# Performance work log

Hardware: AMD Instinct MI355X
Metric: run time of the kernel (lower is better)

Reference implementation:

```python
import jax, jax.numpy as jnp
import numpy as np

D_MODEL, FFN, N_EXP = 1024, 4096, 8
BS, L = 4, 2048


def setup_inputs() -> dict:
    key = jax.random.key(0)
    ks = jax.random.split(key, 7)
    s = 0.02
    return {
        "x": jax.random.normal(ks[0], (BS, L, D_MODEL), dtype=jnp.float32),
        "gate_w": s * jax.random.normal(ks[1], (D_MODEL, N_EXP), dtype=jnp.float32),
        "gate_b": jnp.zeros((N_EXP,), dtype=jnp.float32),
        "W1": s * jax.random.normal(ks[2], (N_EXP, D_MODEL, FFN), dtype=jnp.float32),
        "b1": jnp.zeros((N_EXP, FFN), dtype=jnp.float32),
        "W2": s * jax.random.normal(ks[3], (N_EXP, FFN, D_MODEL), dtype=jnp.float32),
        "b2": jnp.zeros((N_EXP, D_MODEL), dtype=jnp.float32),
    }


def reference(x, gate_w, gate_b, W1, b1, W2, b2):
    # gate logits [bs, l, E]; NOTE: original applies Softmax(dim=1) -> over seq dim
    logits = jnp.einsum("bld,de->ble", x, gate_w) + gate_b
    probs = jax.nn.softmax(logits, axis=1)  # faithful to nn.Softmax(dim=1)
    idx = jnp.argmax(probs, axis=-1)  # top-1 expert per token, [bs, l]
    # topk_weights are computed in the original but never applied to output.
    out = jnp.zeros_like(x)
    for e in range(N_EXP):  # fixed small expert loop (structurally distinct weights)
        h = jax.nn.gelu(jnp.einsum("bld,df->blf", x, W1[e]) + b1[e], approximate=False)
        y = jnp.einsum("blf,fd->bld", h, W2[e]) + b2[e]
        out = out + jnp.where((idx == e)[..., None], y, jnp.float32(0.0))
    return out
```

## Files before the change

kernel.cpp:

```cpp
#include <hip/hip_runtime.h>
#include <hip/hip_bf16.h>

typedef unsigned short u16;
typedef unsigned int u32;

using bf16x8 = __attribute__((ext_vector_type(8))) short;
using f32x4  = __attribute__((ext_vector_type(4))) float;

static constexpr int TOK  = 8192;
static constexpr int SEQ  = 2048;
static constexpr int DM   = 1024;
static constexpr int FF   = 4096;
static constexpr int NE   = 8;
static constexpr int MAXT = 72;
static constexpr int KS2  = 4;
static constexpr int NWG1 = MAXT * (FF/128);
static constexpr int NWG2 = MAXT * (DM/128) * KS2;

static constexpr size_t O_LOGITS = 0;
static constexpr size_t O_M      = 262144;
static constexpr size_t O_Z      = O_M + 128;
static constexpr size_t O_CNT    = O_Z + 128;
static constexpr size_t O_CUR    = O_CNT + 64;
static constexpr size_t O_OFF    = O_CUR + 64;
static constexpr size_t O_DESC   = 263168;
static constexpr size_t O_PERM   = 266240;
static constexpr size_t O_IDX    = 299008;
static constexpr size_t O_XG     = 524288;
static constexpr size_t O_W1T    = O_XG  + (size_t)TOK*DM*2;
static constexpr size_t O_W2T    = O_W1T + (size_t)NE*DM*FF*2;
static constexpr size_t O_H      = O_W2T + (size_t)NE*DM*FF*2;

__device__ __forceinline__ u16 f2bf(float f){
  __hip_bfloat16 h = __float2bfloat16(f);
  return *reinterpret_cast<u16*>(&h);
}

__device__ __forceinline__ void gld_lds16(const void* g, void* l){
  __builtin_amdgcn_global_load_lds((const __attribute__((address_space(1))) void*)g,
                                   (__attribute__((address_space(3))) void*)l, 16, 0, 0);
}

__device__ __forceinline__ float gelu_f(float v){
  float u = v * fmaf(v*v, 0.044715f, 1.0f) * 0.7978845608f;
  float ex = __builtin_amdgcn_exp2f(u * -2.885390082f);
  return v * __builtin_amdgcn_rcpf(1.0f + ex);
}

__global__ void k_gate(const float* __restrict__ x, const float* __restrict__ gw,
                       const float* __restrict__ gb, float* __restrict__ logits){
  __shared__ float sgw[NE*DM];
  for (int i = threadIdx.x; i < DM*NE; i += 256){
    int d = i >> 3, e = i & 7;
    sgw[e*DM + d] = gw[i];
  }
  __syncthreads();
  int wave = threadIdx.x >> 6, lane = threadIdx.x & 63;
  int t = blockIdx.x * 4 + wave;
  const float4* xr = (const float4*)(x + (size_t)t * DM);
  float acc[NE];
#pragma unroll
  for (int e = 0; e < NE; ++e) acc[e] = 0.f;
#pragma unroll
  for (int k = 0; k < 4; ++k){
    int v4 = k*64 + lane;
    float4 v = xr[v4];
#pragma unroll
    for (int e = 0; e < NE; ++e){
      const float4 g = *(const float4*)&sgw[e*DM + v4*4];
      acc[e] = fmaf(v.x, g.x, fmaf(v.y, g.y, fmaf(v.z, g.z, fmaf(v.w, g.w, acc[e]))));
    }
  }
#pragma unroll
  for (int off = 32; off; off >>= 1)
#pragma unroll
    for (int e = 0; e < NE; ++e) acc[e] += __shfl_xor(acc[e], off);
  if (lane == 0){
#pragma unroll
    for (int e = 0; e < NE; ++e) logits[(size_t)t*NE + e] = acc[e] + gb[e];
  }
}

__global__ void k_lse(const float* __restrict__ logits, float* __restrict__ mOut,
                      float* __restrict__ zOut){
  int be = blockIdx.x;
  int b = be >> 3, e = be & 7;
  const float* base = logits + ((size_t)b*SEQ)*NE + e;
  float m = -INFINITY;
  for (int l = threadIdx.x; l < SEQ; l += 256) m = fmaxf(m, base[(size_t)l*NE]);
  __shared__ float red[8];
#pragma unroll
  for (int off = 32; off; off >>= 1) m = fmaxf(m, __shfl_xor(m, off));
  if ((threadIdx.x & 63) == 0) red[threadIdx.x >> 6] = m;
  __syncthreads();
  m = fmaxf(fmaxf(red[0], red[1]), fmaxf(red[2], red[3]));
  float s = 0.f;
  for (int l = threadIdx.x; l < SEQ; l += 256) s += expf(base[(size_t)l*NE] - m);
#pragma unroll
  for (int off = 32; off; off >>= 1) s += __shfl_xor(s, off);
  if ((threadIdx.x & 63) == 0) red[4 + (threadIdx.x >> 6)] = s;
  __syncthreads();
  if (threadIdx.x == 0){ mOut[be] = m; zOut[be] = red[4]+red[5]+red[6]+red[7]; }
}

__global__ void k_route(const float* __restrict__ logits, const float* __restrict__ m,
                        const float* __restrict__ z, u32* __restrict__ cnt,
                        int* __restrict__ idx){
  int t = blockIdx.x*256 + threadIdx.x;
  int b = t >> 11;
  const float* lr = logits + (size_t)t*NE;
  float best = -INFINITY; int be = 0;
#pragma unroll
  for (int e = 0; e < NE; ++e){
    float p = expf(lr[e] - m[b*NE + e]) / z[b*NE + e];
    if (p > best){ best = p; be = e; }
  }
  idx[t] = be;
  atomicAdd(&cnt[be], 1u);
}

__global__ void k_plan(const u32* __restrict__ cnt, int* __restrict__ off,
                       int4* __restrict__ desc, u32* __restrict__ cur){
  if (threadIdx.x == 0){
    int offs[NE+1]; int o = 0;
    for (int e = 0; e < NE; ++e){ offs[e] = o; o += (int)cnt[e]; }
    offs[NE] = o;
    int nt = 0;
    for (int e = 0; e < NE; ++e){
      int c = (int)cnt[e];
      for (int s = 0; s < c; s += 128)
        desc[nt++] = make_int4(e, offs[e] + s, min(128, c - s), 0);
      off[e] = offs[e]; cur[e] = 0u;
    }
    off[NE] = offs[NE];
    for (int i = nt; i < MAXT; ++i) desc[i] = make_int4(-1, 0, 0, 0);
  }
}

__global__ void k_scatter(const int* __restrict__ idx, const int* __restrict__ off,
                          u32* __restrict__ cur, int* __restrict__ perm){
  int t = blockIdx.x*256 + threadIdx.x;
  int e = idx[t];
  int pos = off[e] + (int)atomicAdd(&cur[e], 1u);
  perm[pos] = t;
}

__global__ void k_gather(const float* __restrict__ x, const int* __restrict__ perm,
                         const int* __restrict__ idx, const float* __restrict__ b2,
                         u16* __restrict__ Xg, float* __restrict__ out){
  int p = blockIdx.x;
  int t = perm[p];
  int e = idx[t];
  const float4* src = (const float4*)(x + (size_t)t*DM);
  float4 v = src[threadIdx.x];
  uint2 o;
  o.x = (u32)f2bf(v.x) | ((u32)f2bf(v.y) << 16);
  o.y = (u32)f2bf(v.z) | ((u32)f2bf(v.w) << 16);
  *(uint2*)(Xg + (size_t)p*DM + threadIdx.x*4) = o;
  float4 bv = ((const float4*)(b2 + (size_t)e*DM))[threadIdx.x];
  ((float4*)(out + (size_t)t*DM))[threadIdx.x] = bv;
}

__global__ void k_trans(const float* __restrict__ in, u16* __restrict__ out,
                        int R, int C){
  __shared__ float tile[64][65];
  int e = blockIdx.z;
  int r0 = blockIdx.x*64, c0 = blockIdx.y*64;
  const float* src = in + ((size_t)e*R + r0)*C + c0;
  int lr = threadIdx.x >> 4, lc = (threadIdx.x & 15) * 4;
#pragma unroll
  for (int i = 0; i < 4; ++i){
    float4 v = *(const float4*)(src + (size_t)(lr + i*16)*C + lc);
    tile[lr + i*16][lc+0] = v.x; tile[lr + i*16][lc+1] = v.y;
    tile[lr + i*16][lc+2] = v.z; tile[lr + i*16][lc+3] = v.w;
  }
  __syncthreads();
  u16* dst = out + ((size_t)e*C + c0)*R + r0;
#pragma unroll
  for (int i = 0; i < 4; ++i){
    int oc = lr + i*16;
    u16 a0 = f2bf(tile[lc+0][oc]);
    u16 a1 = f2bf(tile[lc+1][oc]);
    u16 a2 = f2bf(tile[lc+2][oc]);
    u16 a3 = f2bf(tile[lc+3][oc]);
    uint2 o; o.x = (u32)a0 | ((u32)a1 << 16); o.y = (u32)a2 | ((u32)a3 << 16);
    *(uint2*)(dst + (size_t)oc*R + lc) = o;
  }
}


__global__ __launch_bounds__(256) void k_ffn1(const u16* __restrict__ Xg,
    const u16* __restrict__ W1T, const float* __restrict__ b1,
    u16* __restrict__ H, const int4* __restrict__ desc){
  int pid = blockIdx.x;
  int pid_sw = (pid & 7) * (NWG1/8) + (pid >> 3);
  int ng  = pid_sw / (MAXT*8);
  int rem = pid_sw - ng*(MAXT*8);
  int mt  = rem >> 3;
  int n0  = (ng*8 + (rem & 7)) * 128;
  int4 dd = desc[mt];
  int e = dd.x; if (e < 0) return;
  int m0 = dd.y, valid = dd.z;
  __shared__ __align__(16) u16 lA[2][128*32];
  __shared__ __align__(16) u16 lB[2][128*32];
  int tid = threadIdx.x, lane = tid & 63, wave = tid >> 6;
  int wr = wave >> 1, wc = wave & 1;
  const u16* Bsrc = W1T + ((size_t)e*FF + n0)*DM;
  f32x4 acc[4][4] = {};

  auto stage = [&](int buf, int kt){
    int k0 = kt * 32;
#pragma unroll
    for (int i = 0; i < 2; ++i){
      int qbase = wave*512 + i*2048;
      int qe = qbase + lane*8;
      int row = qe >> 5, col = qe & 31;
      int rowg = m0 + row; if (rowg > TOK-1) rowg = TOK-1;
      gld_lds16(Xg + (size_t)rowg*DM + k0 + col, &lA[buf][qbase]);
      gld_lds16(Bsrc + (size_t)row*DM + k0 + col, &lB[buf][qbase]);
    }
  };

  stage(0, 0);
  __syncthreads();
  const int KT = DM / 32;
  for (int kt = 0; kt < KT; ++kt){
    int cur = kt & 1;
    if (kt + 1 < KT) stage(cur ^ 1, kt + 1);
    const u16* pa = &lA[cur][(wr*64 + (lane & 15))*32 + (lane >> 4)*8];
    const u16* pb = &lB[cur][(wc*64 + (lane & 15))*32 + (lane >> 4)*8];
    bf16x8 a[4], b[4];
#pragma unroll
    for (int m = 0; m < 4; ++m) a[m] = *(const bf16x8*)(pa + m*16*32);
#pragma unroll
    for (int n = 0; n < 4; ++n) b[n] = *(const bf16x8*)(pb + n*16*32);
#pragma unroll
    for (int m = 0; m < 4; ++m)
#pragma unroll
      for (int n = 0; n < 4; ++n)
        acc[m][n] = __builtin_amdgcn_mfma_f32_16x16x32_bf16(a[m], b[n], acc[m][n], 0, 0, 0);
    __syncthreads();
  }

#pragma unroll
  for (int n = 0; n < 4; ++n){
    int col = n0 + wc*64 + n*16 + (lane & 15);
    float bias = b1[(size_t)e*FF + col];
#pragma unroll
    for (int m = 0; m < 4; ++m){
      int rbase = wr*64 + m*16 + ((lane >> 4) << 2);
#pragma unroll
      for (int j = 0; j < 4; ++j){
        int rit = rbase + j;
        if (rit < valid){
          float v = acc[m][n][j] + bias;
          H[(size_t)(m0 + rit)*FF + col] = f2bf(gelu_f(v));
        }
      }
    }
  }
}

__global__ __launch_bounds__(256) void k_ffn2(const u16* __restrict__ H,
    const u16* __restrict__ W2T, float* __restrict__ out,
    const int4* __restrict__ desc, const int* __restrict__ perm){
  int pid = blockIdx.x;
  int pid_sw = (pid & 7) * (NWG2/8) + (pid >> 3);
  int ks  = pid_sw / (MAXT*8);
  int rem = pid_sw - ks*(MAXT*8);
  int mt  = rem >> 3;
  int n0  = (rem & 7) * 128;
  int4 dd = desc[mt];
  int e = dd.x; if (e < 0) return;
  int m0 = dd.y, valid = dd.z;
  __shared__ __align__(16) u16 lA[2][128*32];
  __shared__ __align__(16) u16 lB[2][128*32];
  int tid = threadIdx.x, lane = tid & 63, wave = tid >> 6;
  int wr = wave >> 1, wc = wave & 1;
  const u16* Bsrc = W2T + ((size_t)e*DM + n0)*FF;
  const int kbase = ks * (FF/KS2);
  f32x4 acc[4][4] = {};

  auto stage = [&](int buf, int kt){
    int k0 = kbase + kt * 32;
#pragma unroll
    for (int i = 0; i < 2; ++i){
      int qbase = wave*512 + i*2048;
      int qe = qbase + lane*8;
      int row = qe >> 5, col = qe & 31;
      int rowg = m0 + row; if (rowg > TOK-1) rowg = TOK-1;
      gld_lds16(H + (size_t)rowg*FF + k0 + col, &lA[buf][qbase]);
      gld_lds16(Bsrc + (size_t)row*FF + k0 + col, &lB[buf][qbase]);
    }
  };

  stage(0, 0);
  __syncthreads();
  const int KT = (FF/KS2) / 32;
  for (int kt = 0; kt < KT; ++kt){
    int cur = kt & 1;
    if (kt + 1 < KT) stage(cur ^ 1, kt + 1);
    const u16* pa = &lA[cur][(wr*64 + (lane & 15))*32 + (lane >> 4)*8];
    const u16* pb = &lB[cur][(wc*64 + (lane & 15))*32 + (lane >> 4)*8];
    bf16x8 a[4], b[4];
#pragma unroll
    for (int m = 0; m < 4; ++m) a[m] = *(const bf16x8*)(pa + m*16*32);
#pragma unroll
    for (int n = 0; n < 4; ++n) b[n] = *(const bf16x8*)(pb + n*16*32);
#pragma unroll
    for (int m = 0; m < 4; ++m)
#pragma unroll
      for (int n = 0; n < 4; ++n)
        acc[m][n] = __builtin_amdgcn_mfma_f32_16x16x32_bf16(a[m], b[n], acc[m][n], 0, 0, 0);
    __syncthreads();
  }

#pragma unroll
  for (int m = 0; m < 4; ++m){
#pragma unroll
    for (int j = 0; j < 4; ++j){
      int rit = wr*64 + m*16 + ((lane >> 4) << 2) + j;
      if (rit < valid){
        int tok = perm[m0 + rit];
#pragma unroll
        for (int n = 0; n < 4; ++n){
          int col = n0 + wc*64 + n*16 + (lane & 15);
          unsafeAtomicAdd(&out[(size_t)tok*DM + col], acc[m][n][j]);
        }
      }
    }
  }
}

extern "C" void kernel_launch(void* const* d_in, const int* in_sizes, int n_in,
                              void* d_out, int out_size, void* d_ws, size_t ws_size,
                              hipStream_t stream){
  const float* x   = (const float*)d_in[0];
  const float* gw  = (const float*)d_in[1];
  const float* gb  = (const float*)d_in[2];
  const float* W1  = (const float*)d_in[3];
  const float* b1  = (const float*)d_in[4];
  const float* W2  = (const float*)d_in[5];
  const float* b2  = (const float*)d_in[6];
  float* out = (float*)d_out;
  char* ws = (char*)d_ws;

  float* logits = (float*)(ws + O_LOGITS);
  float* mArr   = (float*)(ws + O_M);
  float* zArr   = (float*)(ws + O_Z);
  u32*   cnt    = (u32*)  (ws + O_CNT);
  u32*   cur    = (u32*)  (ws + O_CUR);
  int*   off    = (int*)  (ws + O_OFF);
  int4*  desc   = (int4*) (ws + O_DESC);
  int*   perm   = (int*)  (ws + O_PERM);
  int*   idx    = (int*)  (ws + O_IDX);
  u16*   Xg     = (u16*)  (ws + O_XG);
  u16*   W1T    = (u16*)  (ws + O_W1T);
  u16*   W2T    = (u16*)  (ws + O_W2T);
  u16*   Hbuf   = (u16*)  (ws + O_H);

  hipMemsetAsync(ws + O_CNT, 0, 128, stream);

  k_gate   <<<TOK/4, 256, 0, stream>>>(x, gw, gb, logits);
  k_lse    <<<32,    256, 0, stream>>>(logits, mArr, zArr);
  k_route  <<<TOK/256, 256, 0, stream>>>(logits, mArr, zArr, cnt, idx);
  k_plan   <<<1,     64,  0, stream>>>(cnt, off, desc, cur);
  k_scatter<<<TOK/256, 256, 0, stream>>>(idx, off, cur, perm);
  k_gather <<<TOK,   256, 0, stream>>>(x, perm, idx, b2, Xg, out);
  k_trans  <<<dim3(DM/64, FF/64, NE), 256, 0, stream>>>(W1, W1T, DM, FF);
  k_trans  <<<dim3(FF/64, DM/64, NE), 256, 0, stream>>>(W2, W2T, FF, DM);
  k_ffn1   <<<NWG1,  256, 0, stream>>>(Xg, W1T, b1, Hbuf, desc);
  k_ffn2   <<<NWG2,  256, 0, stream>>>(Hbuf, W2T, out, desc, perm);
}
```

Measured before the change: 510.7 us.

## Triple-buffer swizzled A tiles in LDS and stream B operands directly into registers

Both expert GEMM kernels now stage only the activation tile in LDS. They use a 3-deep ring buffer, a K step of 64 and an XOR swizzle to avoid bank conflicts. The weight operand is read straight from global memory into registers. The per-iteration __syncthreads is replaced by a single s_barrier with a two-stage prefetch distance. MFMA priority is raised via s_setprio, and launch bounds request 3 blocks per CU. This halves LDS traffic and footprint and deepens latency hiding, but it relies on direct global B loads being coalesced enough and on implicit vmcnt ordering for correctness.

```diff
diff --git a/kernel.cpp b/kernel.cpp
--- a/kernel.cpp
+++ b/kernel.cpp
@@ -189,7 +189,7 @@
 }
 
 
-__global__ __launch_bounds__(256) void k_ffn1(const u16* __restrict__ Xg,
+__global__ __launch_bounds__(256, 3) void k_ffn1(const u16* __restrict__ Xg,
     const u16* __restrict__ W1T, const float* __restrict__ b1,
     u16* __restrict__ H, const int4* __restrict__ desc){
   int pid = blockIdx.x;
@@ -201,45 +201,71 @@
   int4 dd = desc[mt];
   int e = dd.x; if (e < 0) return;
   int m0 = dd.y, valid = dd.z;
-  __shared__ __align__(16) u16 lA[2][128*32];
-  __shared__ __align__(16) u16 lB[2][128*32];
+
+  __shared__ __align__(16) u16 lA[3][128*64];
+
   int tid = threadIdx.x, lane = tid & 63, wave = tid >> 6;
   int wr = wave >> 1, wc = wave & 1;
   const u16* Bsrc = W1T + ((size_t)e*FF + n0)*DM;
+
   f32x4 acc[4][4] = {};
-
-  auto stage = [&](int buf, int kt){
-    int k0 = kt * 32;
-#pragma unroll
-    for (int i = 0; i < 2; ++i){
-      int qbase = wave*512 + i*2048;
-      int qe = qbase + lane*8;
-      int row = qe >> 5, col = qe & 31;
-      int rowg = m0 + row; if (rowg > TOK-1) rowg = TOK-1;
-      gld_lds16(Xg + (size_t)rowg*DM + k0 + col, &lA[buf][qbase]);
-      gld_lds16(Bsrc + (size_t)row*DM + k0 + col, &lB[buf][qbase]);
-    }
-  };
-
-  stage(0, 0);
-  __syncthreads();
-  const int KT = DM / 32;
+  bf16x8 a[4][2], b[4][2];
+
+  int srow = lane >> 3;
+  int cole = ((lane & 7) ^ srow) << 3;
+
+  const u16* rowp[4];
+#pragma unroll
+  for (int g = 0; g < 4; ++g)
+    rowp[g] = Bsrc + (size_t)(wc*64 + g*16 + (lane & 15))*DM + (lane >> 4)*8;
+
+  auto STAGE = [&](int buf, int kt){
+    int k0 = kt * 64;
+    char* dA = (char*)&lA[buf][0];
+#pragma unroll
+    for (int c = 0; c < 4; ++c){
+      int ci = wave*4 + c;
+      int row = ci*8 + srow;
+      int ra = m0 + row; if (ra > TOK-1) ra = TOK-1;
+      gld_lds16(Xg + (size_t)ra*DM + k0 + cole, dA + ci*1024);
+    }
+  };
+  auto LDB = [&](int kt){
+#pragma unroll
+    for (int g = 0; g < 4; ++g){
+      b[g][0] = *(const bf16x8*)(rowp[g] + kt*64);
+      b[g][1] = *(const bf16x8*)(rowp[g] + kt*64 + 32);
+    }
+  };
+  auto LDA = [&](const u16* tb){
+#pragma unroll
+    for (int f = 0; f < 4; ++f){
+      int R = wr*64 + f*16 + (lane & 15);
+      int base = R*128 + (((lane >> 4)*16) ^ ((R & 7) << 4));
+      a[f][0] = *(const bf16x8*)((const char*)tb + base);
+      a[f][1] = *(const bf16x8*)((const char*)tb + (base ^ 64));
+    }
+  };
+
+  STAGE(0, 0);
+  STAGE(1, 1);
+  asm volatile("s_waitcnt vmcnt(4)");
+  __builtin_amdgcn_sched_barrier(0);
+  const int KT = DM / 64;
   for (int kt = 0; kt < KT; ++kt){
-    int cur = kt & 1;
-    if (kt + 1 < KT) stage(cur ^ 1, kt + 1);
-    const u16* pa = &lA[cur][(wr*64 + (lane & 15))*32 + (lane >> 4)*8];
-    const u16* pb = &lB[cur][(wc*64 + (lane & 15))*32 + (lane >> 4)*8];
-    bf16x8 a[4], b[4];
-#pragma unroll
-    for (int m = 0; m < 4; ++m) a[m] = *(const bf16x8*)(pa + m*16*32);
-#pragma unroll
-    for (int n = 0; n < 4; ++n) b[n] = *(const bf16x8*)(pb + n*16*32);
+    __builtin_amdgcn_s_barrier();
+    LDB(kt);
+    if (kt + 2 < KT) STAGE((kt + 2) % 3, kt + 2);
+    LDA(&lA[kt % 3][0]);
+    __builtin_amdgcn_s_setprio(1);
 #pragma unroll
     for (int m = 0; m < 4; ++m)
 #pragma unroll
-      for (int n = 0; n < 4; ++n)
-        acc[m][n] = __builtin_amdgcn_mfma_f32_16x16x32_bf16(a[m], b[n], acc[m][n], 0, 0, 0);
-    __syncthreads();
+      for (int n = 0; n < 4; ++n){
+        acc[m][n] = __builtin_amdgcn_mfma_f32_16x16x32_bf16(a[m][0], b[n][0], acc[m][n], 0,0,0);
+        acc[m][n] = __builtin_amdgcn_mfma_f32_16x16x32_bf16(a[m][1], b[n][1], acc[m][n], 0,0,0);
+      }
+    __builtin_amdgcn_s_setprio(0);
   }
 
 #pragma unroll
@@ -261,7 +287,7 @@
   }
 }
 
-__global__ __launch_bounds__(256) void k_ffn2(const u16* __restrict__ H,
+__global__ __launch_bounds__(256, 3) void k_ffn2(const u16* __restrict__ H,
     const u16* __restrict__ W2T, float* __restrict__ out,
     const int4* __restrict__ desc, const int* __restrict__ perm){
   int pid = blockIdx.x;
@@ -273,46 +299,72 @@
   int4 dd = desc[mt];
   int e = dd.x; if (e < 0) return;
   int m0 = dd.y, valid = dd.z;
-  __shared__ __align__(16) u16 lA[2][128*32];
-  __shared__ __align__(16) u16 lB[2][128*32];
+
+  __shared__ __align__(16) u16 lA[3][128*64];
+
   int tid = threadIdx.x, lane = tid & 63, wave = tid >> 6;
   int wr = wave >> 1, wc = wave & 1;
   const u16* Bsrc = W2T + ((size_t)e*DM + n0)*FF;
   const int kbase = ks * (FF/KS2);
+
   f32x4 acc[4][4] = {};
-
-  auto stage = [&](int buf, int kt){
-    int k0 = kbase + kt * 32;
-#pragma unroll
-    for (int i = 0; i < 2; ++i){
-      int qbase = wave*512 + i*2048;
-      int qe = qbase + lane*8;
-      int row = qe >> 5, col = qe & 31;
-      int rowg = m0 + row; if (rowg > TOK-1) rowg = TOK-1;
-      gld_lds16(H + (size_t)rowg*FF + k0 + col, &lA[buf][qbase]);
-      gld_lds16(Bsrc + (size_t)row*FF + k0 + col, &lB[buf][qbase]);
-    }
-  };
-
-  stage(0, 0);
-  __syncthreads();
-  const int KT = (FF/KS2) / 32;
+  bf16x8 a[4][2], b[4][2];
+
+  int srow = lane >> 3;
+  int cole = ((lane & 7) ^ srow) << 3;
+
+  const u16* rowp[4];
+#pragma unroll
+  for (int g = 0; g < 4; ++g)
+    rowp[g] = Bsrc + (size_t)(wc*64 + g*16 + (lane & 15))*FF + kbase + (lane >> 4)*8;
+
+  auto STAGE = [&](int buf, int kt){
+    int k0 = kbase + kt * 64;
+    char* dA = (char*)&lA[buf][0];
+#pragma unroll
+    for (int c = 0; c < 4; ++c){
+      int ci = wave*4 + c;
+      int row = ci*8 + srow;
+      int ra = m0 + row; if (ra > TOK-1) ra = TOK-1;
+      gld_lds16(H + (size_t)ra*FF + k0 + cole, dA + ci*1024);
+    }
+  };
+  auto LDB = [&](int kt){
+#pragma unroll
+    for (int g = 0; g < 4; ++g){
+      b[g][0] = *(const bf16x8*)(rowp[g] + kt*64);
+      b[g][1] = *(const bf16x8*)(rowp[g] + kt*64 + 32);
+    }
+  };
+  auto LDA = [&](const u16* tb){
+#pragma unroll
+    for (int f = 0; f < 4; ++f){
+      int R = wr*64 + f*16 + (lane & 15);
+      int base = R*128 + (((lane >> 4)*16) ^ ((R & 7) << 4));
+      a[f][0] = *(const bf16x8*)((const char*)tb + base);
+      a[f][1] = *(const bf16x8*)((const char*)tb + (base ^ 64));
+    }
+  };
+
+  STAGE(0, 0);
+  STAGE(1, 1);
+  asm volatile("s_waitcnt vmcnt(4)");
+  __builtin_amdgcn_sched_barrier(0);
+  const int KT = (FF/KS2) / 64;
   for (int kt = 0; kt < KT; ++kt){
-    int cur = kt & 1;
-    if (kt + 1 < KT) stage(cur ^ 1, kt + 1);
-    const u16* pa = &lA[cur][(wr*64 + (lane & 15))*32 + (lane >> 4)*8];
-    const u16* pb = &lB[cur][(wc*64 + (lane & 15))*32 + (lane >> 4)*8];
-    bf16x8 a[4], b[4];
-#pragma unroll
-    for (int m = 0; m < 4; ++m) a[m] = *(const bf16x8*)(pa + m*16*32);
-#pragma unroll
-    for (int n = 0; n < 4; ++n) b[n] = *(const bf16x8*)(pb + n*16*32);
+    __builtin_amdgcn_s_barrier();
+    LDB(kt);
+    if (kt + 2 < KT) STAGE((kt + 2) % 3, kt + 2);
+    LDA(&lA[kt % 3][0]);
+    __builtin_amdgcn_s_setprio(1);
 #pragma unroll
     for (int m = 0; m < 4; ++m)
 #pragma unroll
-      for (int n = 0; n < 4; ++n)
-        acc[m][n] = __builtin_amdgcn_mfma_f32_16x16x32_bf16(a[m], b[n], acc[m][n], 0, 0, 0);
-    __syncthreads();
+      for (int n = 0; n < 4; ++n){
+        acc[m][n] = __builtin_amdgcn_mfma_f32_16x16x32_bf16(a[m][0], b[n][0], acc[m][n], 0,0,0);
+        acc[m][n] = __builtin_amdgcn_mfma_f32_16x16x32_bf16(a[m][1], b[n][1], acc[m][n], 0,0,0);
+      }
+    __builtin_amdgcn_s_setprio(0);
   }
 
 #pragma unroll
```

Result: slower. 604.0 us (+18.3%).

## Use 8-wave workgroups in expert GEMMs and widen transpose stores

Applied to the files above, without the earlier changes.

The expert FFN GEMM kernels now launch 512 threads (8 waves) per 128x128 tile, so each wave covers a 32x64 sub-tile instead of 64x64. This halves the accumulator registers per wave, with the aim of more waves in flight to hide latency, and each thread now stages one 16-byte chunk of A and of B per k-step. The trade-off is that each wave issues fewer MFMAs per LDS load. Separately, the weight transpose kernel writes 8 bf16 values per thread as 16-byte stores instead of 4 values as 8-byte stores, aiming for wider global writes.

```diff
diff --git a/kernel.cpp b/kernel.cpp
--- a/kernel.cpp
+++ b/kernel.cpp
@@ -176,20 +176,25 @@
   }
   __syncthreads();
   u16* dst = out + ((size_t)e*C + c0)*R + r0;
-#pragma unroll
-  for (int i = 0; i < 4; ++i){
-    int oc = lr + i*16;
-    u16 a0 = f2bf(tile[lc+0][oc]);
-    u16 a1 = f2bf(tile[lc+1][oc]);
-    u16 a2 = f2bf(tile[lc+2][oc]);
-    u16 a3 = f2bf(tile[lc+3][oc]);
-    uint2 o; o.x = (u32)a0 | ((u32)a1 << 16); o.y = (u32)a2 | ((u32)a3 << 16);
-    *(uint2*)(dst + (size_t)oc*R + lc) = o;
-  }
-}
-
-
-__global__ __launch_bounds__(256) void k_ffn1(const u16* __restrict__ Xg,
+  int rr = (threadIdx.x & 7) * 8;
+  int ocb = threadIdx.x >> 3;
+#pragma unroll
+  for (int p = 0; p < 2; ++p){
+    int oc = ocb + p*32;
+    u16 w[8];
+#pragma unroll
+    for (int k = 0; k < 8; ++k) w[k] = f2bf(tile[rr + k][oc]);
+    uint4 o;
+    o.x = (u32)w[0] | ((u32)w[1] << 16);
+    o.y = (u32)w[2] | ((u32)w[3] << 16);
+    o.z = (u32)w[4] | ((u32)w[5] << 16);
+    o.w = (u32)w[6] | ((u32)w[7] << 16);
+    *(uint4*)(dst + (size_t)oc*R + rr) = o;
+  }
+}
+
+
+__global__ __launch_bounds__(512) void k_ffn1(const u16* __restrict__ Xg,
     const u16* __restrict__ W1T, const float* __restrict__ b1,
     u16* __restrict__ H, const int4* __restrict__ desc){
   int pid = blockIdx.x;
@@ -206,19 +211,15 @@
   int tid = threadIdx.x, lane = tid & 63, wave = tid >> 6;
   int wr = wave >> 1, wc = wave & 1;
   const u16* Bsrc = W1T + ((size_t)e*FF + n0)*DM;
-  f32x4 acc[4][4] = {};
-
+  f32x4 acc[2][4] = {};
+
+  int srow = tid >> 2;
+  int scol = (tid & 3) * 8;
   auto stage = [&](int buf, int kt){
     int k0 = kt * 32;
-#pragma unroll
-    for (int i = 0; i < 2; ++i){
-      int qbase = wave*512 + i*2048;
-      int qe = qbase + lane*8;
-      int row = qe >> 5, col = qe & 31;
-      int rowg = m0 + row; if (rowg > TOK-1) rowg = TOK-1;
-      gld_lds16(Xg + (size_t)rowg*DM + k0 + col, &lA[buf][qbase]);
-      gld_lds16(Bsrc + (size_t)row*DM + k0 + col, &lB[buf][qbase]);
-    }
+    int ra = m0 + srow; if (ra > TOK-1) ra = TOK-1;
+    gld_lds16(Xg   + (size_t)ra  *DM + k0 + scol, &lA[buf][tid*8]);
+    gld_lds16(Bsrc + (size_t)srow*DM + k0 + scol, &lB[buf][tid*8]);
   };
 
   stage(0, 0);
@@ -227,15 +228,15 @@
   for (int kt = 0; kt < KT; ++kt){
     int cur = kt & 1;
     if (kt + 1 < KT) stage(cur ^ 1, kt + 1);
-    const u16* pa = &lA[cur][(wr*64 + (lane & 15))*32 + (lane >> 4)*8];
+    const u16* pa = &lA[cur][(wr*32 + (lane & 15))*32 + (lane >> 4)*8];
     const u16* pb = &lB[cur][(wc*64 + (lane & 15))*32 + (lane >> 4)*8];
-    bf16x8 a[4], b[4];
-#pragma unroll
-    for (int m = 0; m < 4; ++m) a[m] = *(const bf16x8*)(pa + m*16*32);
+    bf16x8 a[2], b[4];
+#pragma unroll
+    for (int m = 0; m < 2; ++m) a[m] = *(const bf16x8*)(pa + m*16*32);
 #pragma unroll
     for (int n = 0; n < 4; ++n) b[n] = *(const bf16x8*)(pb + n*16*32);
 #pragma unroll
-    for (int m = 0; m < 4; ++m)
+    for (int m = 0; m < 2; ++m)
 #pragma unroll
       for (int n = 0; n < 4; ++n)
         acc[m][n] = __builtin_amdgcn_mfma_f32_16x16x32_bf16(a[m], b[n], acc[m][n], 0, 0, 0);
@@ -247,8 +248,8 @@
     int col = n0 + wc*64 + n*16 + (lane & 15);
     float bias = b1[(size_t)e*FF + col];
 #pragma unroll
-    for (int m = 0; m < 4; ++m){
-      int rbase = wr*64 + m*16 + ((lane >> 4) << 2);
+    for (int m = 0; m < 2; ++m){
+      int rbase = wr*32 + m*16 + ((lane >> 4) << 2);
 #pragma unroll
       for (int j = 0; j < 4; ++j){
         int rit = rbase + j;
@@ -261,7 +262,7 @@
   }
 }
 
-__global__ __launch_bounds__(256) void k_ffn2(const u16* __restrict__ H,
+__global__ __launch_bounds__(512) void k_ffn2(const u16* __restrict__ H,
     const u16* __restrict__ W2T, float* __restrict__ out,
     const int4* __restrict__ desc, const int* __restrict__ perm){
   int pid = blockIdx.x;
@@ -279,19 +280,15 @@
   int wr = wave >> 1, wc = wave & 1;
   const u16* Bsrc = W2T + ((size_t)e*DM + n0)*FF;
   const int kbase = ks * (FF/KS2);
-  f32x4 acc[4][4] = {};
-
+  f32x4 acc[2][4] = {};
+
+  int srow = tid >> 2;
+  int scol = (tid & 3) * 8;
   auto stage = [&](int buf, int kt){
     int k0 = kbase + kt * 32;
-#pragma unroll
-    for (int i = 0; i < 2; ++i){
-      int qbase = wave*512 + i*2048;
-      int qe = qbase + lane*8;
-      int row = qe >> 5, col = qe & 31;
-      int rowg = m0 + row; if (rowg > TOK-1) rowg = TOK-1;
-      gld_lds16(H + (size_t)rowg*FF + k0 + col, &lA[buf][qbase]);
-      gld_lds16(Bsrc + (size_t)row*FF + k0 + col, &lB[buf][qbase]);
-    }
+    int ra = m0 + srow; if (ra > TOK-1) ra = TOK-1;
+    gld_lds16(H    + (size_t)ra  *FF + k0 + scol, &lA[buf][tid*8]);
+    gld_lds16(Bsrc + (size_t)srow*FF + k0 + scol, &lB[buf][tid*8]);
   };
 
   stage(0, 0);
@@ -300,15 +297,15 @@
   for (int kt = 0; kt < KT; ++kt){
     int cur = kt & 1;
     if (kt + 1 < KT) stage(cur ^ 1, kt + 1);
-    const u16* pa = &lA[cur][(wr*64 + (lane & 15))*32 + (lane >> 4)*8];
+    const u16* pa = &lA[cur][(wr*32 + (lane & 15))*32 + (lane >> 4)*8];
     const u16* pb = &lB[cur][(wc*64 + (lane & 15))*32 + (lane >> 4)*8];
-    bf16x8 a[4], b[4];
-#pragma unroll
-    for (int m = 0; m < 4; ++m) a[m] = *(const bf16x8*)(pa + m*16*32);
+    bf16x8 a[2], b[4];
+#pragma unroll
+    for (int m = 0; m < 2; ++m) a[m] = *(const bf16x8*)(pa + m*16*32);
 #pragma unroll
     for (int n = 0; n < 4; ++n) b[n] = *(const bf16x8*)(pb + n*16*32);
 #pragma unroll
-    for (int m = 0; m < 4; ++m)
+    for (int m = 0; m < 2; ++m)
 #pragma unroll
       for (int n = 0; n < 4; ++n)
         acc[m][n] = __builtin_amdgcn_mfma_f32_16x16x32_bf16(a[m], b[n], acc[m][n], 0, 0, 0);
@@ -316,10 +313,10 @@
   }
 
 #pragma unroll
-  for (int m = 0; m < 4; ++m){
+  for (int m = 0; m < 2; ++m){
 #pragma unroll
     for (int j = 0; j < 4; ++j){
-      int rit = wr*64 + m*16 + ((lane >> 4) << 2) + j;
+      int rit = wr*32 + m*16 + ((lane >> 4) << 2) + j;
       if (rit < valid){
         int tok = perm[m0 + rit];
 #pragma unroll
@@ -369,6 +366,6 @@
   k_gather <<<TOK,   256, 0, stream>>>(x, perm, idx, b2, Xg, out);
   k_trans  <<<dim3(DM/64, FF/64, NE), 256, 0, stream>>>(W1, W1T, DM, FF);
   k_trans  <<<dim3(FF/64, DM/64, NE), 256, 0, stream>>>(W2, W2T, FF, DM);
-  k_ffn1   <<<NWG1,  256, 0, stream>>>(Xg, W1T, b1, Hbuf, desc);
-  k_ffn2   <<<NWG2,  256, 0, stream>>>(Hbuf, W2T, out, desc, perm);
-}
+  k_ffn1   <<<NWG1,  512, 0, stream>>>(Xg, W1T, b1, Hbuf, desc);
+  k_ffn2   <<<NWG2,  512, 0, stream>>>(Hbuf, W2T, out, desc, perm);
+}
```

Measured after the change: 482.9 us. 5.4% less time.
